# Optimization experiments

Measured on AMD Instinct MI355X. Metric: run time of the kernel, lower is better.

## Reference

```python
import jax, jax.numpy as jnp
import numpy as np
from jax import lax

DROPOUT_RATE = 0.1  # config['dropout']


def setup_inputs() -> dict:
    key = jax.random.key(0)
    kx, kl, kwi, kwh = jax.random.split(key, 4)
    B, T, D, H = 64, 2048, 256, 256
    datamat = jax.random.normal(kx, (B, T, D), dtype=jnp.float32)
    datalens = jax.random.randint(kl, (B,), 1, T + 1, dtype=jnp.int32)
    # OptimizedLSTMCell params: combined input/hidden kernels, gate order (i, f, g, o)
    s_i = 1.0 / np.sqrt(D)
    s_h = 1.0 / np.sqrt(H)
    Wi = jax.random.uniform(kwi, (D, 4 * H), jnp.float32, -s_i, s_i)
    Wh = jax.random.uniform(kwh, (H, 4 * H), jnp.float32, -s_h, s_h)
    b = jnp.zeros((4 * H,), dtype=jnp.float32)
    return {"datamat": datamat, "Wi": Wi, "Wh": Wh, "b": b, "datalens": datalens}


def _dropout(x, rate):
    # training=True dropout with a fixed key (deterministic reference)
    keep = jax.random.bernoulli(jax.random.key(42), 1.0 - rate, x.shape)
    return jnp.where(keep, x / (1.0 - rate), jnp.zeros_like(x))


def _lstm_forward(x, Wi, Wh, b, datalens):
    # x: [B, T, D]
    B, T, D = x.shape
    H = Wh.shape[0]

    def step(carry, xt):
        c, h = carry
        z = xt @ Wi + h @ Wh + b  # [B, 4H], gate order i, f, g, o
        i, f, g, o = jnp.split(z, 4, axis=-1)
        c_new = jax.nn.sigmoid(f) * c + jax.nn.sigmoid(i) * jnp.tanh(g)
        h_new = jax.nn.sigmoid(o) * jnp.tanh(c_new)
        return (c_new, h_new), (c_new, h_new)

    c0 = jnp.zeros((B, H), dtype=x.dtype)
    h0 = jnp.zeros((B, H), dtype=x.dtype)
    _, (cs, hs) = lax.scan(step, (c0, h0), jnp.swapaxes(x, 0, 1))  # [T, B, H] each
    outputs = jnp.swapaxes(hs, 0, 1)  # [B, T, H]
    # flax nn.RNN with seq_lengths + return_carry: select carry at t = len-1 per batch
    idx = jnp.clip(datalens.astype(jnp.int32) - 1, 0, T - 1)  # [B]
    bidx = jnp.arange(B)
    c_last = cs[idx, bidx]  # [B, H]
    h_last = hs[idx, bidx]  # [B, H]
    return (c_last, h_last), outputs


def reference(datamat, Wi, Wh, b, datalens):
    x = _dropout(datamat, DROPOUT_RATE)
    out_carry, outputs = _lstm_forward(x, Wi, Wh, b, datalens)
    return (out_carry, outputs)
```

## Files before the change

### kernel.cpp

```cpp
#include <hip/hip_runtime.h>


typedef __attribute__((ext_vector_type(8))) short short8;
typedef __attribute__((ext_vector_type(4))) float floatx4;
typedef __attribute__((ext_vector_type(4))) int int4v;
typedef __attribute__((ext_vector_type(4))) unsigned short us4;

__device__ __forceinline__ unsigned short f2bf(float f) {
  unsigned int u = __float_as_uint(f);
  u = u + 0x7fffu + ((u >> 16) & 1u);
  return (unsigned short)(u >> 16);
}
__device__ __forceinline__ float bf2f(unsigned short s) {
  return __uint_as_float(((unsigned int)s) << 16);
}
__device__ __forceinline__ float fexp2(float x) { return __builtin_amdgcn_exp2f(x); }
__device__ __forceinline__ float frcp(float x) { return __builtin_amdgcn_rcpf(x); }

__device__ __forceinline__ unsigned int tf_bits(unsigned int x0, unsigned int x1) {
  const unsigned int K0 = 0u, K1 = 42u;
  const unsigned int KX = K0 ^ K1 ^ 0x1BD11BDAu;
  x0 += K0; x1 += K1;
#define TF_R(r) { x0 += x1; x1 = (x1 << (r)) | (x1 >> (32 - (r))); x1 ^= x0; }
  TF_R(13) TF_R(15) TF_R(26) TF_R(6)   x0 += K1; x1 += KX + 1u;
  TF_R(17) TF_R(29) TF_R(16) TF_R(24)  x0 += KX; x1 += K0 + 2u;
  TF_R(13) TF_R(15) TF_R(26) TF_R(6)   x0 += K0; x1 += K1 + 3u;
  TF_R(17) TF_R(29) TF_R(16) TF_R(24)  x0 += K1; x1 += KX + 4u;
  TF_R(13) TF_R(15) TF_R(26) TF_R(6)   x0 += KX; x1 += K0 + 5u;
#undef TF_R
  return x0 ^ x1;
}

__global__ __launch_bounds__(256) void k_dropout(const float* __restrict__ x,
                                                 unsigned short* __restrict__ xd) {
  const unsigned int base = (blockIdx.x * 256u + threadIdx.x) * 4u;
  const float4 xv = *reinterpret_cast<const float4*>(x + base);
  const float xs[4] = {xv.x, xv.y, xv.z, xv.w};
  us4 o;
#pragma unroll
  for (int j = 0; j < 4; ++j) {
    const unsigned int bits = tf_bits(0u, base + (unsigned int)j);
    const float u = __uint_as_float((bits >> 9) | 0x3f800000u) - 1.0f;
    const float v = (u < 0.9f) ? (xs[j] / 0.9f) : 0.0f;
    o[j] = f2bf(v);
  }
  *reinterpret_cast<us4*>(xd + base) = o;
}

__global__ __launch_bounds__(256) void k_pack_wi(const float* __restrict__ wi,
                                                 unsigned short* __restrict__ wit) {
  const int tid = blockIdx.x * 256 + threadIdx.x;
  const int n = tid >> 8, k = tid & 255;
  wit[n * 256 + k] = f2bf(wi[k * 1024 + n]);
}

__global__ __launch_bounds__(256) void k_colscale(const float* __restrict__ wh,
                                                  float* __restrict__ dq,
                                                  float* __restrict__ qs) {
  const int n = blockIdx.x * 256 + threadIdx.x;
  float m = 0.f;
  for (int k = 0; k < 256; ++k) m = fmaxf(m, fabsf(wh[k * 1024 + n]));
  const float s = (m > 0.f) ? m : 1.f;
  dq[n] = s / 16129.0f;
  qs[n] = 127.0f / s;
}

__global__ __launch_bounds__(256) void k_pack_wh_i8(const float* __restrict__ wh,
                                                    const float* __restrict__ qs,
                                                    signed char* __restrict__ wq) {
  const int tid = blockIdx.x * 256 + threadIdx.x;
  const int j = tid & 15, l = (tid >> 4) & 63, kt = (tid >> 10) & 3, ntg = tid >> 12;
  const int k = kt * 64 + ((l >> 4) << 4) + j;
  const int n = ntg * 16 + (l & 15);
  float v = rintf(wh[k * 1024 + n] * qs[n]);
  v = fminf(fmaxf(v, -127.f), 127.f);
  wq[tid] = (signed char)(int)v;
}

__global__ __launch_bounds__(256) void k_gemm_x(const unsigned short* __restrict__ xd,
                                                const unsigned short* __restrict__ wit,
                                                const float* __restrict__ bias,
                                                unsigned short* __restrict__ xp) {
  __shared__ unsigned short SH[20480];
  const int tid = threadIdx.x;
  const int lane = tid & 63;
  const int wv = tid >> 6;
  const int wm = wv >> 1, wn = wv & 1;
  const int m0 = blockIdx.x * 128;
  const int y = blockIdx.y;

  const int srow = tid >> 1, sseg = tid & 1;
  const unsigned short* gA = xd + (m0 + srow) * 256 + sseg * 16;
  const int nsrc = ((srow >> 5) << 8) + y * 32 + (srow & 31);
  const unsigned short* gB = wit + nsrc * 256 + sseg * 16;
  const int soff = srow * 40 + sseg * 16;

  const floatx4 zero4 = {0.f, 0.f, 0.f, 0.f};
  floatx4 acc[4][4];
#pragma unroll
  for (int i = 0; i < 4; ++i)
#pragma unroll
    for (int j = 0; j < 4; ++j) acc[i][j] = zero4;

  short8 ra0 = *(const short8*)(gA);
  short8 ra1 = *(const short8*)(gA + 8);
  short8 rb0 = *(const short8*)(gB);
  short8 rb1 = *(const short8*)(gB + 8);
  *(short8*)&SH[soff] = ra0;
  *(short8*)&SH[soff + 8] = ra1;
  *(short8*)&SH[10240 + soff] = rb0;
  *(short8*)&SH[10240 + soff + 8] = rb1;
  __syncthreads();

  const int frow = (lane & 15) * 40 + ((lane >> 4) << 3);
#pragma unroll 1
  for (int kt = 0; kt < 8; ++kt) {
    const int boff = (kt & 1) * 5120;
    if (kt < 7) {
      ra0 = *(const short8*)(gA + (kt + 1) * 32);
      ra1 = *(const short8*)(gA + (kt + 1) * 32 + 8);
      rb0 = *(const short8*)(gB + (kt + 1) * 32);
      rb1 = *(const short8*)(gB + (kt + 1) * 32 + 8);
    }
    short8 af[4], bfv[4];
#pragma unroll
    for (int mt = 0; mt < 4; ++mt)
      af[mt] = *(const short8*)&SH[boff + (wm * 64 + mt * 16) * 40 + frow];
#pragma unroll
    for (int nt = 0; nt < 4; ++nt)
      bfv[nt] = *(const short8*)&SH[10240 + boff + (wn * 64 + nt * 16) * 40 + frow];
#pragma unroll
    for (int mt = 0; mt < 4; ++mt)
#pragma unroll
      for (int nt = 0; nt < 4; ++nt)
        acc[mt][nt] = __builtin_amdgcn_mfma_f32_16x16x32_bf16(af[mt], bfv[nt], acc[mt][nt], 0, 0, 0);
    if (kt < 7) {
      const int noff = (boff ^ 5120);
      *(short8*)&SH[noff + soff] = ra0;
      *(short8*)&SH[noff + soff + 8] = ra1;
      *(short8*)&SH[10240 + noff + soff] = rb0;
      *(short8*)&SH[10240 + noff + soff + 8] = rb1;
    }
    __syncthreads();
  }

  float bv[4];
#pragma unroll
  for (int nt = 0; nt < 4; ++nt)
    bv[nt] = bias[((wn * 2 + (nt >> 1)) << 8) + y * 32 + ((nt & 1) << 4) + (lane & 15)];

  __syncthreads();
#pragma unroll
  for (int mt = 0; mt < 4; ++mt) {
#pragma unroll
    for (int nt = 0; nt < 4; ++nt) {
      const int jj = wn * 64 + nt * 16 + (lane & 15);
#pragma unroll
      for (int q = 0; q < 4; ++q) {
        const int row = wm * 64 + mt * 16 + ((lane >> 4) << 2) + q;
        SH[row * 132 + jj] = f2bf(acc[mt][nt][q] + bv[nt]);
      }
    }
  }
  __syncthreads();

#pragma unroll
  for (int k = 0; k < 16; ++k) {
    const int pi = k * 256 + tid;
    const int row = pi >> 5, u = pi & 31;
    us4 o = {SH[row * 132 + u], SH[row * 132 + 32 + u],
             SH[row * 132 + 64 + u], SH[row * 132 + 96 + u]};
    const int m = m0 + row;
    *(us4*)(xp + ((size_t)(m & 2047) * 64 + (m >> 11)) * 1024 +
            (size_t)(y * 32 + u) * 4) = o;
  }
}

__global__ __launch_bounds__(512, 2) void k_lstm(const unsigned short* __restrict__ xp,
                                                 const signed char* __restrict__ wq,
                                                 const float* __restrict__ dq,
                                                 const int* __restrict__ lens,
                                                 float* __restrict__ out) {
  __shared__ __align__(16) signed char As[8192];

  const int tid = threadIdx.x, lane = tid & 63, v = tid >> 6;
  const int wg = blockIdx.x, b0 = wg * 2;

  const int4v zacc = {0, 0, 0, 0};
  ((int4v*)As)[tid] = zacc;

  int4v w[4][2][4];
#pragma unroll
  for (int g = 0; g < 4; ++g)
#pragma unroll
    for (int p = 0; p < 2; ++p)
#pragma unroll
      for (int kt = 0; kt < 4; ++kt) {
        const int ntg = g * 16 + v * 2 + p;
        w[g][p][kt] = *(const int4v*)(wq + (size_t)(((ntg * 4 + kt) * 64 + lane)) * 16);
      }

  const int r = (lane >> 4) & 1;
  const int ph = lane >> 5;
  const int u = v * 32 + ph * 16 + (lane & 15);

  float dqv[4];
#pragma unroll
  for (int g = 0; g < 4; ++g) dqv[g] = dq[g * 256 + u];
  const int lenm = lens[b0 + r] - 1;
  float c = 0.f;

  const int aw0 = (u >> 6) * 1024 + (((u >> 4) & 3) * 16 + r * 4) * 16 + (u & 15);
  const int aw1 = aw0 + 128;

  const unsigned short* px = xp + (size_t)(b0 + r) * 1024 + u * 4;
  float* po = out + 32768 + (size_t)(b0 + r) * 2048 * 256 + u;
  float* pc = out + (size_t)(b0 + r) * 256 + u;
  float* phl = pc + 16384;

  us4 xc = *(const us4*)px;
  px += 65536;

  __syncthreads();

  int curoff = 0;
  const float LOG2E = 1.44269504f;

#pragma unroll 1
  for (int t = 0; t < 2048; ++t) {
    const us4 xn = *(const us4*)px;
    px += 65536;

    int4v af0 = *(const int4v*)&As[curoff + lane * 16];
    int4v af1 = *(const int4v*)&As[curoff + 1024 + lane * 16];
    int4v af2 = *(const int4v*)&As[curoff + 2048 + lane * 16];
    int4v af3 = *(const int4v*)&As[curoff + 3072 + lane * 16];

    int4v acc[4][2];
#pragma unroll
    for (int g = 0; g < 4; ++g)
#pragma unroll
      for (int p = 0; p < 2; ++p) {
        acc[g][p] = __builtin_amdgcn_mfma_i32_16x16x64_i8(af0, w[g][p][0], zacc, 0, 0, 0);
        acc[g][p] = __builtin_amdgcn_mfma_i32_16x16x64_i8(af1, w[g][p][1], acc[g][p], 0, 0, 0);
        acc[g][p] = __builtin_amdgcn_mfma_i32_16x16x64_i8(af2, w[g][p][2], acc[g][p], 0, 0, 0);
        acc[g][p] = __builtin_amdgcn_mfma_i32_16x16x64_i8(af3, w[g][p][3], acc[g][p], 0, 0, 0);
      }

    float z[4];
#pragma unroll
    for (int g = 0; g < 4; ++g) {
      const int zint = (ph == 0) ? acc[g][0][0] : acc[g][1][0];
      z[g] = fmaf((float)zint, dqv[g], bf2f(xc[g]));
    }
    const float zi_ = fminf(fmaxf(z[0], -20.f), 20.f);
    const float zf_ = fminf(fmaxf(z[1], -20.f), 20.f);
    const float zg_ = fminf(fmaxf(z[2], -20.f), 20.f);
    const float zo_ = fminf(fmaxf(z[3], -20.f), 20.f);
    const float ei = fexp2(zi_ * LOG2E);
    const float e2g = fexp2(zg_ * (2.f * LOG2E));
    const float p1 = ei * (e2g - 1.f) * frcp((ei + 1.f) * (e2g + 1.f));
    const float ef = fexp2(-zf_ * LOG2E);
    const float cn = frcp(1.f + ef) * c + p1;
    c = cn;
    const float cc = fminf(fmaxf(cn, -15.f), 15.f);
    const float eo = fexp2(zo_ * LOG2E);
    const float e2c = fexp2(cc * (2.f * LOG2E));
    const float h = eo * (e2c - 1.f) * frcp((eo + 1.f) * (e2c + 1.f));

    float hq = rintf(h * 127.f);
    hq = fminf(fmaxf(hq, -127.f), 127.f);
    const signed char hb = (signed char)(int)hq;
    const int woff = curoff ^ 4096;
    As[woff + aw0] = hb;
    As[woff + aw1] = hb;

    *po = h;
    po += 256;
    if (t == lenm) {
      *pc = cn;
      *phl = h;
    }

    xc = xn;
    __syncthreads();
    curoff ^= 4096;
  }
}

extern "C" void kernel_launch(void* const* d_in, const int* in_sizes, int n_in,
                              void* d_out, int out_size, void* d_ws, size_t ws_size,
                              hipStream_t stream) {
  (void)in_sizes; (void)n_in; (void)out_size; (void)ws_size;
  const float* x = (const float*)d_in[0];
  const float* wi = (const float*)d_in[1];
  const float* wh = (const float*)d_in[2];
  const float* bias = (const float*)d_in[3];
  const int* lens = (const int*)d_in[4];
  float* out = (float*)d_out;

  char* ws = (char*)d_ws;
  unsigned short* xd = (unsigned short*)ws;
  unsigned short* xp = (unsigned short*)(ws + 67108864ull);
  unsigned short* wit = (unsigned short*)(ws + 335544320ull);
  float* dq = (float*)(ws + 336068608ull);
  float* qs = (float*)(ws + 336072704ull);
  signed char* wqb = (signed char*)(ws + 336076800ull);

  k_pack_wi<<<1024, 256, 0, stream>>>(wi, wit);
  k_colscale<<<4, 256, 0, stream>>>(wh, dq, qs);
  k_pack_wh_i8<<<1024, 256, 0, stream>>>(wh, qs, wqb);
  k_dropout<<<32768, 256, 0, stream>>>(x, xd);
  k_gemm_x<<<dim3(1024, 8), 256, 0, stream>>>(xd, wit, bias, xp);
  k_lstm<<<32, 512, 0, stream>>>(xp, wqb, dq, lens, out);
}
```

Measured before the change: 1.641 ms.

## Fold exp2 gate scaling into precomputed weights and unroll LSTM loop by two

Pre-multiplies the log2e and sign and double factors for each gate into the dequant scales and the input-projection output, so the recurrent loop feeds exp2 directly without per-gate multiplies or two-sided clamps. The time loop is unrolled by two with constant LDS double-buffer offsets, uses a magic-number float-to-int trick for h quantization, and defers the last-carry stores until after the loop. The weight-pack and column-scale prep kernels are rewritten to use coalesced shared-memory transposes and reductions. Dropping the lower clamps and the h saturation leans on exp2 and rcp handling large values correctly. Scaling before bf16 rounding also changes precision slightly.

Measured after the change: 1.542 ms. -6.1%, faster.

```diff
diff --git a/kernel.cpp b/kernel.cpp
--- a/kernel.cpp
+++ b/kernel.cpp
@@ -6,13 +6,12 @@
 typedef __attribute__((ext_vector_type(4))) int int4v;
 typedef __attribute__((ext_vector_type(4))) unsigned short us4;
 
+#define LOG2E 1.44269504088896f
+
 __device__ __forceinline__ unsigned short f2bf(float f) {
   unsigned int u = __float_as_uint(f);
   u = u + 0x7fffu + ((u >> 16) & 1u);
   return (unsigned short)(u >> 16);
-}
-__device__ __forceinline__ float bf2f(unsigned short s) {
-  return __uint_as_float(((unsigned int)s) << 16);
 }
 __device__ __forceinline__ float fexp2(float x) { return __builtin_amdgcn_exp2f(x); }
 __device__ __forceinline__ float frcp(float x) { return __builtin_amdgcn_rcpf(x); }
@@ -49,20 +48,41 @@
 
 __global__ __launch_bounds__(256) void k_pack_wi(const float* __restrict__ wi,
                                                  unsigned short* __restrict__ wit) {
-  const int tid = blockIdx.x * 256 + threadIdx.x;
-  const int n = tid >> 8, k = tid & 255;
-  wit[n * 256 + k] = f2bf(wi[k * 1024 + n]);
+  __shared__ float tile[32][33];
+  const int k0 = blockIdx.x * 32, n0 = blockIdx.y * 32;
+  const int tx = threadIdx.x & 31, ty = threadIdx.x >> 5;
+#pragma unroll
+  for (int i = 0; i < 4; ++i)
+    tile[ty + i * 8][tx] = wi[(k0 + ty + i * 8) * 1024 + n0 + tx];
+  __syncthreads();
+#pragma unroll
+  for (int i = 0; i < 4; ++i)
+    wit[(n0 + ty + i * 8) * 256 + k0 + tx] = f2bf(tile[tx][ty + i * 8]);
 }
 
 __global__ __launch_bounds__(256) void k_colscale(const float* __restrict__ wh,
                                                   float* __restrict__ dq,
                                                   float* __restrict__ qs) {
-  const int n = blockIdx.x * 256 + threadIdx.x;
+  __shared__ float red[256];
+  const int t = threadIdx.x;
+  const int n = blockIdx.x * 16 + (t & 15);
+  const int kg = t >> 4;
   float m = 0.f;
-  for (int k = 0; k < 256; ++k) m = fmaxf(m, fabsf(wh[k * 1024 + n]));
-  const float s = (m > 0.f) ? m : 1.f;
-  dq[n] = s / 16129.0f;
-  qs[n] = 127.0f / s;
+#pragma unroll
+  for (int i = 0; i < 16; ++i)
+    m = fmaxf(m, fabsf(wh[(kg * 16 + i) * 1024 + n]));
+  red[t] = m;
+  __syncthreads();
+  if (t < 16) {
+    const int nn = blockIdx.x * 16 + t;
+    float mm = red[t];
+#pragma unroll
+    for (int j = 1; j < 16; ++j) mm = fmaxf(mm, red[t + j * 16]);
+    const float s = (mm > 0.f) ? mm : 1.f;
+    const float gsc[4] = {LOG2E, -LOG2E, 2.f * LOG2E, LOG2E};
+    dq[nn] = (s / 16129.0f) * gsc[nn >> 8];
+    qs[nn] = 127.0f / s;
+  }
 }
 
 __global__ __launch_bounds__(256) void k_pack_wh_i8(const float* __restrict__ wh,
@@ -144,10 +164,14 @@
     __syncthreads();
   }
 
-  float bv[4];
-#pragma unroll
-  for (int nt = 0; nt < 4; ++nt)
-    bv[nt] = bias[((wn * 2 + (nt >> 1)) << 8) + y * 32 + ((nt & 1) << 4) + (lane & 15)];
+  const float gsc[4] = {LOG2E, -LOG2E, 2.f * LOG2E, LOG2E};
+  float bv[4], gv[4];
+#pragma unroll
+  for (int nt = 0; nt < 4; ++nt) {
+    const int gate = wn * 2 + (nt >> 1);
+    bv[nt] = bias[(gate << 8) + y * 32 + ((nt & 1) << 4) + (lane & 15)];
+    gv[nt] = gsc[gate];
+  }
 
   __syncthreads();
 #pragma unroll
@@ -158,7 +182,7 @@
 #pragma unroll
       for (int q = 0; q < 4; ++q) {
         const int row = wm * 64 + mt * 16 + ((lane >> 4) << 2) + q;
-        SH[row * 132 + jj] = f2bf(acc[mt][nt][q] + bv[nt]);
+        SH[row * 132 + jj] = f2bf((acc[mt][nt][q] + bv[nt]) * gv[nt]);
       }
     }
   }
@@ -204,88 +228,96 @@
   const int ph = lane >> 5;
   const int u = v * 32 + ph * 16 + (lane & 15);
 
-  float dqv[4];
-#pragma unroll
-  for (int g = 0; g < 4; ++g) dqv[g] = dq[g * 256 + u];
+  float dq0 = dq[u], dq1 = dq[256 + u], dq2 = dq[512 + u], dq3 = dq[768 + u];
   const int lenm = lens[b0 + r] - 1;
-  float c = 0.f;
-
-  const int aw0 = (u >> 6) * 1024 + (((u >> 4) & 3) * 16 + r * 4) * 16 + (u & 15);
-  const int aw1 = aw0 + 128;
-
-  const unsigned short* px = xp + (size_t)(b0 + r) * 1024 + u * 4;
-  float* po = out + 32768 + (size_t)(b0 + r) * 2048 * 256 + u;
-  float* pc = out + (size_t)(b0 + r) * 256 + u;
-  float* phl = pc + 16384;
-
-  us4 xc = *(const us4*)px;
-  px += 65536;
-
-  __syncthreads();
-
-  int curoff = 0;
-  const float LOG2E = 1.44269504f;
+  float c = 0.f, ckeep = 0.f, hkeep = 0.f;
+
+  const signed char* AsR = As + lane * 16;
+  signed char* AsW = As + ((u >> 6) * 1024 + (((u >> 4) & 3) * 16 + r * 4) * 16 + (u & 15));
+
+  const char* xpb = (const char*)xp;
+  unsigned int xoff = ((unsigned int)(b0 + r) * 1024u + (unsigned int)u * 4u) * 2u;
+  char* outb = (char*)(out + 32768);
+  unsigned int ooff = ((unsigned int)(b0 + r) * 524288u + (unsigned int)u) * 4u;
+
+  uint2 xc = *(const uint2*)(xpb + xoff);
+  xoff += 131072u;
+
+  __syncthreads();
+
+#define GATES(XPAIR, WOFF0, WOFF1)                                              \
+  {                                                                             \
+    const float xi = __uint_as_float(XPAIR.x << 16);                            \
+    const float xf = __uint_as_float(XPAIR.x & 0xffff0000u);                    \
+    const float xg = __uint_as_float(XPAIR.y << 16);                            \
+    const float xo = __uint_as_float(XPAIR.y & 0xffff0000u);                    \
+    const int ai = ph ? acc[0][1][0] : acc[0][0][0];                            \
+    const int af_ = ph ? acc[1][1][0] : acc[1][0][0];                           \
+    const int ag = ph ? acc[2][1][0] : acc[2][0][0];                            \
+    const int ao = ph ? acc[3][1][0] : acc[3][0][0];                            \
+    const float zi = fminf(fmaf((float)ai, dq0, xi), 28.85f);                   \
+    const float zf = fmaf((float)af_, dq1, xf);                                 \
+    const float zg = fminf(fmaf((float)ag, dq2, xg), 57.71f);                   \
+    const float zo = fminf(fmaf((float)ao, dq3, xo), 28.85f);                   \
+    const float ei = fexp2(zi);                                                 \
+    const float e2g = fexp2(zg);                                                \
+    const float ef = fexp2(zf);                                                 \
+    const float eo = fexp2(zo);                                                 \
+    const float p1 = ei * (e2g - 1.f) * frcp((ei + 1.f) * (e2g + 1.f));         \
+    const float cn = fmaf(frcp(1.f + ef), c, p1);                               \
+    c = cn;                                                                     \
+    const float e2c = fexp2(fminf(cn, 15.f) * (2.f * LOG2E));                   \
+    const float h = eo * (e2c - 1.f) * frcp((eo + 1.f) * (e2c + 1.f));          \
+    const float hm = fmaf(h, 127.f, 12582912.f);                                \
+    AsW[WOFF0] = (signed char)__float_as_uint(hm);                              \
+    AsW[WOFF1] = (signed char)__float_as_uint(hm);                              \
+    *(float*)(outb + ooff) = h;                                                 \
+    ooff += 1024u;                                                              \
+    if (t_ == lenm) { ckeep = cn; hkeep = h; }                                  \
+  }
+
+#define MFMA_BLOCK(O0, O1, O2, O3)                                              \
+  int4v acc[4][2];                                                              \
+  {                                                                             \
+    const int4v a0 = *(const int4v*)(AsR + (O0));                               \
+    const int4v a1 = *(const int4v*)(AsR + (O1));                               \
+    const int4v a2 = *(const int4v*)(AsR + (O2));                               \
+    const int4v a3 = *(const int4v*)(AsR + (O3));                               \
+    _Pragma("unroll") for (int g = 0; g < 4; ++g)                               \
+    _Pragma("unroll") for (int p = 0; p < 2; ++p) {                             \
+      acc[g][p] = __builtin_amdgcn_mfma_i32_16x16x64_i8(a0, w[g][p][0], zacc, 0, 0, 0); \
+      acc[g][p] = __builtin_amdgcn_mfma_i32_16x16x64_i8(a1, w[g][p][1], acc[g][p], 0, 0, 0); \
+      acc[g][p] = __builtin_amdgcn_mfma_i32_16x16x64_i8(a2, w[g][p][2], acc[g][p], 0, 0, 0); \
+      acc[g][p] = __builtin_amdgcn_mfma_i32_16x16x64_i8(a3, w[g][p][3], acc[g][p], 0, 0, 0); \
+    }                                                                           \
+  }
 
 #pragma unroll 1
-  for (int t = 0; t < 2048; ++t) {
-    const us4 xn = *(const us4*)px;
-    px += 65536;
-
-    int4v af0 = *(const int4v*)&As[curoff + lane * 16];
-    int4v af1 = *(const int4v*)&As[curoff + 1024 + lane * 16];
-    int4v af2 = *(const int4v*)&As[curoff + 2048 + lane * 16];
-    int4v af3 = *(const int4v*)&As[curoff + 3072 + lane * 16];
-
-    int4v acc[4][2];
-#pragma unroll
-    for (int g = 0; g < 4; ++g)
-#pragma unroll
-      for (int p = 0; p < 2; ++p) {
-        acc[g][p] = __builtin_amdgcn_mfma_i32_16x16x64_i8(af0, w[g][p][0], zacc, 0, 0, 0);
-        acc[g][p] = __builtin_amdgcn_mfma_i32_16x16x64_i8(af1, w[g][p][1], acc[g][p], 0, 0, 0);
-        acc[g][p] = __builtin_amdgcn_mfma_i32_16x16x64_i8(af2, w[g][p][2], acc[g][p], 0, 0, 0);
-        acc[g][p] = __builtin_amdgcn_mfma_i32_16x16x64_i8(af3, w[g][p][3], acc[g][p], 0, 0, 0);
-      }
-
-    float z[4];
-#pragma unroll
-    for (int g = 0; g < 4; ++g) {
-      const int zint = (ph == 0) ? acc[g][0][0] : acc[g][1][0];
-      z[g] = fmaf((float)zint, dqv[g], bf2f(xc[g]));
-    }
-    const float zi_ = fminf(fmaxf(z[0], -20.f), 20.f);
-    const float zf_ = fminf(fmaxf(z[1], -20.f), 20.f);
-    const float zg_ = fminf(fmaxf(z[2], -20.f), 20.f);
-    const float zo_ = fminf(fmaxf(z[3], -20.f), 20.f);
-    const float ei = fexp2(zi_ * LOG2E);
-    const float e2g = fexp2(zg_ * (2.f * LOG2E));
-    const float p1 = ei * (e2g - 1.f) * frcp((ei + 1.f) * (e2g + 1.f));
-    const float ef = fexp2(-zf_ * LOG2E);
-    const float cn = frcp(1.f + ef) * c + p1;
-    c = cn;
-    const float cc = fminf(fmaxf(cn, -15.f), 15.f);
-    const float eo = fexp2(zo_ * LOG2E);
-    const float e2c = fexp2(cc * (2.f * LOG2E));
-    const float h = eo * (e2c - 1.f) * frcp((eo + 1.f) * (e2c + 1.f));
-
-    float hq = rintf(h * 127.f);
-    hq = fminf(fmaxf(hq, -127.f), 127.f);
-    const signed char hb = (signed char)(int)hq;
-    const int woff = curoff ^ 4096;
-    As[woff + aw0] = hb;
-    As[woff + aw1] = hb;
-
-    *po = h;
-    po += 256;
-    if (t == lenm) {
-      *pc = cn;
-      *phl = h;
-    }
-
-    xc = xn;
-    __syncthreads();
-    curoff ^= 4096;
-  }
+  for (int it = 0; it < 1024; ++it) {
+    {
+      const int t_ = 2 * it;
+      const uint2 xn = *(const uint2*)(xpb + xoff);
+      xoff += 131072u;
+      MFMA_BLOCK(0, 1024, 2048, 3072)
+      GATES(xc, 4096, 4224)
+      xc = xn;
+      __syncthreads();
+    }
+    {
+      const int t_ = 2 * it + 1;
+      const uint2 xn = *(const uint2*)(xpb + xoff);
+      xoff += 131072u;
+      MFMA_BLOCK(4096, 5120, 6144, 7168)
+      GATES(xc, 0, 128)
+      xc = xn;
+      __syncthreads();
+    }
+  }
+#undef GATES
+#undef MFMA_BLOCK
+
+  out[(size_t)(b0 + r) * 256 + u] = ckeep;
+  out[16384 + (size_t)(b0 + r) * 256 + u] = hkeep;
 }
 
 extern "C" void kernel_launch(void* const* d_in, const int* in_sizes, int n_in,
@@ -307,8 +339,8 @@
   float* qs = (float*)(ws + 336072704ull);
   signed char* wqb = (signed char*)(ws + 336076800ull);
 
-  k_pack_wi<<<1024, 256, 0, stream>>>(wi, wit);
-  k_colscale<<<4, 256, 0, stream>>>(wh, dq, qs);
+  k_pack_wi<<<dim3(8, 32), 256, 0, stream>>>(wi, wit);
+  k_colscale<<<64, 256, 0, stream>>>(wh, dq, qs);
   k_pack_wh_i8<<<1024, 256, 0, stream>>>(wh, qs, wqb);
   k_dropout<<<32768, 256, 0, stream>>>(x, xd);
   k_gemm_x<<<dim3(1024, 8), 256, 0, stream>>>(xd, wit, bias, xp);
```
